# Kernel optimization log

Measured on AMD Instinct MI355X. Metric: run time of the kernel, lower is better.

## Reference

```python
import jax, jax.numpy as jnp
import numpy as np

N = 50000
E = 500000
D = 128      # input_nf = output_nf = hidden_nf
EPS = 1e-8
MAX_TRANS = 10.0


def setup_inputs() -> dict:
    key = jax.random.key(0)
    ks = jax.random.split(key, 16)
    s = lambda k, shp: jax.random.normal(k, shp, dtype=jnp.float32) * 0.05
    inp = {
        "h": jax.random.normal(ks[0], (N, D), dtype=jnp.float32),
        "edge_index": jax.random.randint(ks[1], (2, E), 0, N, dtype=jnp.int64),
        "coord": jax.random.normal(ks[2], (N, 3), dtype=jnp.float32),
        # edge_mlp: Linear(2D+1 -> D), SiLU, Linear(D -> D), SiLU
        "We1": s(ks[3], (2 * D + 1, D)), "be1": jnp.zeros((D,), jnp.float32),
        "We2": s(ks[4], (D, D)),         "be2": jnp.zeros((D,), jnp.float32),
        # att_mlp: Linear(D -> 1), Sigmoid
        "Watt": s(ks[5], (D, 1)), "batt": jnp.zeros((1,), jnp.float32),
        # coord_mlp: Linear(D -> D), SiLU, Linear(D -> 1, bias=False, xavier gain=0.001)
        "Wc1": s(ks[6], (D, D)), "bc1": jnp.zeros((D,), jnp.float32),
        "Wc2": s(ks[7], (D, 1)) * 0.001,
        # node_mlp: Linear(2D -> D), SiLU, Linear(D -> D)
        "Wn1": s(ks[8], (2 * D, D)), "bn1": jnp.zeros((D,), jnp.float32),
        "Wn2": s(ks[9], (D, D)),     "bn2": jnp.zeros((D,), jnp.float32),
    }
    return inp


def _segment_mean(data, seg_ids, num_segments):
    tot = jax.ops.segment_sum(data, seg_ids, num_segments=num_segments)
    cnt = jax.ops.segment_sum(jnp.ones_like(data), seg_ids, num_segments=num_segments)
    return tot / jnp.clip(cnt, 1.0, None)


def reference(h, edge_index, coord, We1, be1, We2, be2, Watt, batt,
              Wc1, bc1, Wc2, Wn1, bn1, Wn2, bn2):
    row, col = edge_index[0], edge_index[1]

    # coord2radial (normalize=False)
    coord_diff = coord[row] - coord[col]                      # [E, 3]
    radial = jnp.sum(coord_diff ** 2, axis=1, keepdims=True)  # [E, 1]

    # edge_model with attention
    e_in = jnp.concatenate([h[row], h[col], radial], axis=1)  # [E, 2D+1]
    e = jax.nn.silu(e_in @ We1 + be1)
    edge_feat = jax.nn.silu(e @ We2 + be2)                    # [E, D]
    att = jax.nn.sigmoid(edge_feat @ Watt + batt)             # [E, 1]
    edge_feat = edge_feat * att

    # coord_model (update_coords=True, coords_agg='mean', tanh=False)
    cw = jax.nn.silu(edge_feat @ Wc1 + bc1) @ Wc2             # [E, 1]
    trans = jnp.clip(coord_diff * cw, -MAX_TRANS, MAX_TRANS)  # [E, 3]
    agg_c = jnp.clip(_segment_mean(trans, row, N), -MAX_TRANS, MAX_TRANS)
    coord_out = coord + agg_c

    # node_model (residual=True)
    agg = jax.ops.segment_sum(edge_feat, row, num_segments=N)  # [N, D]
    n_in = jnp.concatenate([h, agg], axis=1)                   # [N, 2D]
    h_out = h + (jax.nn.silu(n_in @ Wn1 + bn1) @ Wn2 + bn2)

    return h_out, coord_out, edge_feat
```

## Files before the change

### kernel.cpp

```cpp
#include <hip/hip_runtime.h>

typedef unsigned short ushort_t;
typedef __attribute__((ext_vector_type(8))) short short8;
typedef __attribute__((ext_vector_type(4))) float f32x4;

#define NN 50000
#define EE 500000
#define DD 128
#define MAXT 10.0f

#define MFMA(a,b,c) __builtin_amdgcn_mfma_f32_16x16x32_bf16((a),(b),(c),0,0,0)

__device__ __forceinline__ ushort_t f2bf(float x){
  unsigned u = __float_as_uint(x);
  u += 0x7FFFu + ((u>>16)&1u);
  return (ushort_t)(u>>16);
}
__device__ __forceinline__ float sigm(float x){ return 1.0f/(1.0f+__expf(-x)); }
__device__ __forceinline__ float siluf(float x){ return x*sigm(x); }
__device__ __forceinline__ float clamp10(float x){ return fminf(fmaxf(x,-MAXT),MAXT); }

__device__ __forceinline__ short8 ldcvt(const float* p){
  f32x4 x = *(const f32x4*)p;
  f32x4 y = *(const f32x4*)(p+4);
  short8 t;
  #pragma unroll
  for (int j=0;j<4;++j){ t[j]=(short)f2bf(x[j]); t[j+4]=(short)f2bf(y[j]); }
  return t;
}

__global__ void k_prep(const float* __restrict__ We1, const float* __restrict__ We2,
                       const float* __restrict__ Wc1, const float* __restrict__ Wn1,
                       const float* __restrict__ Wn2, ushort_t* __restrict__ wpre)
{
  int idx = blockIdx.x*256 + threadIdx.x;
  if (idx >= 7*16384) return;
  int mat = idx >> 14;
  int loc = idx & 16383;
  int n = loc >> 7;
  int kidx = loc & 127;
  int ko = 16*(kidx&7) + (kidx>>3);
  float v;
  switch(mat){
    case 0: v = We1[kidx*DD + n]; break;
    case 1: v = We1[(128+kidx)*DD + n]; break;
    case 2: v = We2[ko*DD + n]; break;
    case 3: v = Wc1[ko*DD + n]; break;
    case 4: v = Wn1[kidx*DD + n]; break;
    case 5: v = Wn1[(128+kidx)*DD + n]; break;
    default: v = Wn2[ko*DD + n]; break;
  }
  int byteoff = n*256 + ((kidx*2) ^ ((n&7)<<4));
  *(ushort_t*)((char*)wpre + (size_t)mat*32768 + byteoff) = f2bf(v);
}

__global__ void k_zero(int* __restrict__ cnt){
  int i = blockIdx.x*256 + threadIdx.x;
  if (i < NN) cnt[i] = 0;
}
__global__ void k_count(const int* __restrict__ eidx, int* __restrict__ cnt){
  int e = blockIdx.x*256 + threadIdx.x;
  if (e < EE) atomicAdd(&cnt[eidx[e]], 1);
}
#define SCAN_B 196
__global__ void k_bsum(const int* __restrict__ cnt, int* __restrict__ bsum){
  __shared__ int sh[256];
  int t = threadIdx.x;
  int i = blockIdx.x*256 + t;
  sh[t] = (i < NN) ? cnt[i] : 0;
  __syncthreads();
  for (int off=128; off>0; off>>=1){
    if (t < off) sh[t] += sh[t+off];
    __syncthreads();
  }
  if (t==0) bsum[blockIdx.x] = sh[0];
}
__global__ void k_bscan(const int* __restrict__ bsum, int* __restrict__ boff){
  __shared__ int sh[256];
  int t = threadIdx.x;
  sh[t] = (t < SCAN_B) ? bsum[t] : 0;
  __syncthreads();
  for (int off=1; off<256; off<<=1){
    int x = (t>=off) ? sh[t-off] : 0;
    __syncthreads();
    sh[t] += x;
    __syncthreads();
  }
  if (t < SCAN_B) boff[t] = (t>0) ? sh[t-1] : 0;
}
__global__ void k_rscan(const int* __restrict__ cnt, const int* __restrict__ boff,
                        int* __restrict__ rowstart, int* __restrict__ cursor){
  __shared__ int sh[256];
  int t = threadIdx.x;
  int i = blockIdx.x*256 + t;
  int v = (i < NN) ? cnt[i] : 0;
  sh[t] = v;
  __syncthreads();
  for (int off=1; off<256; off<<=1){
    int x = (t>=off) ? sh[t-off] : 0;
    __syncthreads();
    sh[t] += x;
    __syncthreads();
  }
  int excl = sh[t] - v + boff[blockIdx.x];
  if (i < NN){ rowstart[i] = excl; cursor[i] = excl; }
  if (i == 0) rowstart[NN] = EE;
}
__global__ void k_scatter(const int* __restrict__ eidx, int* __restrict__ cursor,
                          int* __restrict__ csr){
  int e = blockIdx.x*256 + threadIdx.x;
  if (e < EE){
    int p = atomicAdd(&cursor[eidx[e]], 1);
    csr[p] = e;
  }
}

__device__ __forceinline__ void gemm_lds8(const ushort_t* ebuf, const ushort_t* Wbuf,
                                          int wv, int q, int s, f32x4 acc[8])
{
  #pragma unroll
  for (int kc=0;kc<4;++kc){
    const int koff = ((kc*64+q*16) ^ ((s&7)<<4));
    short8 a0 = *(const short8*)((const char*)ebuf + (wv*16+s)*256 + koff);
    #pragma unroll
    for (int ct=0;ct<8;++ct){
      short8 bf = *(const short8*)((const char*)Wbuf + (ct*16+s)*256 + koff);
      acc[ct] = MFMA(a0,bf,acc[ct]);
    }
  }
}
__device__ __forceinline__ void gemm_regA8(const short8 af[4], const ushort_t* Wbuf,
                                           int q, int s, f32x4 acc[8])
{
  #pragma unroll
  for (int kc=0;kc<4;++kc){
    const int koff = ((kc*64+q*16) ^ ((s&7)<<4));
    #pragma unroll
    for (int ct=0;ct<8;++ct){
      short8 bf = *(const short8*)((const char*)Wbuf + (ct*16+s)*256 + koff);
      acc[ct] = MFMA(af[kc],bf,acc[ct]);
    }
  }
}
__device__ __forceinline__ void zacc8(f32x4 acc[8]){
  #pragma unroll
  for (int b=0;b<8;++b) acc[b] = (f32x4){0.f,0.f,0.f,0.f};
}

__launch_bounds__(512,4)
__global__ void k_edge(const float* __restrict__ h,
                       const int* __restrict__ eidx,
                       const float* __restrict__ coord,
                       const float* __restrict__ We1,
                       const float* __restrict__ be1,
                       const float* __restrict__ be2,
                       const float* __restrict__ Watt,
                       const float* __restrict__ batt,
                       const float* __restrict__ bc1,
                       const float* __restrict__ Wc2,
                       const ushort_t* __restrict__ wpre,
                       float* __restrict__ ef_out,
                       float* __restrict__ trans)
{
  __shared__ ushort_t Wbuf[16384];
  __shared__ ushort_t ebuf[16384];
  const int tid = threadIdx.x;
  const int wv = tid>>6, ln = tid&63;
  const int q = ln>>4, s = ln&15;
  const int we0 = blockIdx.x*128 + wv*16;
  const int* rowI = eidx;
  const int* colI = eidx + EE;

  const int eM = min(we0 + (ln&15), EE-1);
  const int rM = rowI[eM], cM = colI[eM];
  const float cdx = coord[rM*3+0]-coord[cM*3+0];
  const float cdy = coord[rM*3+1]-coord[cM*3+1];
  const float cdz = coord[rM*3+2]-coord[cM*3+2];
  const float radial = cdx*cdx+cdy*cdy+cdz*cdz;

  const int eS0 = min(we0 + s, EE-1);
  const int nR0 = rowI[eS0], nC0 = colI[eS0];

  f32x4 acc[8];
  zacc8(acc);
  short8 af[4];

  #pragma unroll
  for (int kc=0;kc<4;++kc)
    af[kc] = ldcvt(h + (size_t)nR0*DD + kc*32 + q*8);
  { const f32x4* src=(const f32x4*)(wpre); f32x4* dst=(f32x4*)Wbuf;
    #pragma unroll
    for(int i=0;i<4;++i) dst[tid+512*i]=src[tid+512*i]; }
  __syncthreads();
  gemm_regA8(af, Wbuf, q, s, acc);

  #pragma unroll
  for (int kc=0;kc<4;++kc)
    af[kc] = ldcvt(h + (size_t)nC0*DD + kc*32 + q*8);
  __syncthreads();
  { const f32x4* src=(const f32x4*)(wpre+16384); f32x4* dst=(f32x4*)Wbuf;
    #pragma unroll
    for(int i=0;i<4;++i) dst[tid+512*i]=src[tid+512*i]; }
  __syncthreads();
  gemm_regA8(af, Wbuf, q, s, acc);

  {
    float wr[8], bb[8];
    #pragma unroll
    for (int t=0;t<8;++t){ wr[t]=We1[256*DD + 16*t+s]; bb[t]=be1[16*t+s]; }
    #pragma unroll
    for (int r=0;r<4;++r){
      int mloc = q*4 + r;
      float rad = __shfl(radial, mloc);
      short8 pk;
      #pragma unroll
      for (int t=0;t<8;++t){
        float v = siluf(acc[t][r] + rad*wr[t] + bb[t]);
        pk[t]=(short)f2bf(v);
      }
      int m = wv*16 + mloc;
      *(short8*)((char*)ebuf + m*256 + ((s*16) ^ ((m&7)<<4))) = pk;
    }
  }
  zacc8(acc);
  __syncthreads();
  { const f32x4* src=(const f32x4*)(wpre+2*16384); f32x4* dst=(f32x4*)Wbuf;
    #pragma unroll
    for(int i=0;i<4;++i) dst[tid+512*i]=src[tid+512*i]; }
  __syncthreads();

  gemm_lds8(ebuf, Wbuf, wv, q, s, acc);
  {
    float wa[8], bb[8];
    #pragma unroll
    for (int t=0;t<8;++t){ wa[t]=Watt[16*t+s]; bb[t]=be2[16*t+s]; }
    const float bat = batt[0];
    #pragma unroll
    for (int r=0;r<4;++r){
      #pragma unroll
      for (int t=0;t<8;++t) acc[t][r] = siluf(acc[t][r] + bb[t]);
      float p=0.f;
      #pragma unroll
      for (int t=0;t<8;++t) p += acc[t][r]*wa[t];
      p += __shfl_xor(p,1); p += __shfl_xor(p,2);
      p += __shfl_xor(p,4); p += __shfl_xor(p,8);
      const float att = sigm(p + bat);
      #pragma unroll
      for (int t=0;t<8;++t) acc[t][r] *= att;
    }
    #pragma unroll
    for (int r=0;r<4;++r){
      int mloc = q*4 + r;
      int e = we0 + mloc;
      short8 pk;
      #pragma unroll
      for (int t=0;t<8;++t) pk[t]=(short)f2bf(acc[t][r]);
      int m = wv*16 + mloc;
      *(short8*)((char*)ebuf + m*256 + ((s*16) ^ ((m&7)<<4))) = pk;
      if (e < EE){
        float* rp = ef_out + (size_t)e*DD + s;
        #pragma unroll
        for (int t=0;t<8;++t) rp[16*t] = acc[t][r];
      }
    }
  }
  zacc8(acc);
  __syncthreads();
  { const f32x4* src=(const f32x4*)(wpre+3*16384); f32x4* dst=(f32x4*)Wbuf;
    #pragma unroll
    for(int i=0;i<4;++i) dst[tid+512*i]=src[tid+512*i]; }
  __syncthreads();

  gemm_lds8(ebuf, Wbuf, wv, q, s, acc);
  {
    float wc[8], bb[8];
    #pragma unroll
    for (int t=0;t<8;++t){ wc[t]=Wc2[16*t+s]; bb[t]=bc1[16*t+s]; }
    #pragma unroll
    for (int r=0;r<4;++r){
      float p=0.f;
      #pragma unroll
      for (int t=0;t<8;++t) p += siluf(acc[t][r]+bb[t])*wc[t];
      p += __shfl_xor(p,1); p += __shfl_xor(p,2);
      p += __shfl_xor(p,4); p += __shfl_xor(p,8);
      int mloc = q*4 + r;
      int e = we0 + mloc;
      float dx = __shfl(cdx, mloc), dy = __shfl(cdy, mloc), dz = __shfl(cdz, mloc);
      if (e < EE && s == 0){
        trans[(size_t)e*3+0] = clamp10(dx*p);
        trans[(size_t)e*3+1] = clamp10(dy*p);
        trans[(size_t)e*3+2] = clamp10(dz*p);
      }
    }
  }
}

__launch_bounds__(256)
__global__ void k_agg(const float* __restrict__ ef,
                      const float* __restrict__ trans,
                      const int* __restrict__ rowstart,
                      const int* __restrict__ csr,
                      const float* __restrict__ coord,
                      float* __restrict__ agg,
                      float* __restrict__ coord_out)
{
  const int wv = threadIdx.x>>6, ln = threadIdx.x&63;
  const int n = blockIdx.x*4 + wv;
  if (n >= NN) return;
  const int rs = rowstart[n], re = rowstart[n+1];
  const int deg = re - rs;
  const int half = ln>>5, l4 = (ln&31)*4;
  float a0=0,a1=0,a2=0,a3=0;
  for (int j=half; j<deg; j+=2){
    const float* p = ef + (size_t)csr[rs+j]*DD + l4;
    f32x4 v = *(const f32x4*)p;
    a0+=v[0]; a1+=v[1]; a2+=v[2]; a3+=v[3];
  }
  a0 += __shfl_xor(a0,32); a1 += __shfl_xor(a1,32);
  a2 += __shfl_xor(a2,32); a3 += __shfl_xor(a3,32);
  if (half==0){
    f32x4 o = {a0,a1,a2,a3};
    *(f32x4*)(agg + (size_t)n*DD + l4) = o;
  }
  float tx=0,ty=0,tz=0;
  for (int j=ln;j<deg;j+=64){
    const float* t = trans + (size_t)csr[rs+j]*3;
    tx+=t[0]; ty+=t[1]; tz+=t[2];
  }
  #pragma unroll
  for (int m=1;m<64;m<<=1){
    tx+=__shfl_xor(tx,m); ty+=__shfl_xor(ty,m); tz+=__shfl_xor(tz,m);
  }
  if (ln==0){
    const float inv = 1.0f/(float)max(deg,1);
    coord_out[(size_t)n*3+0] = coord[(size_t)n*3+0] + clamp10(tx*inv);
    coord_out[(size_t)n*3+1] = coord[(size_t)n*3+1] + clamp10(ty*inv);
    coord_out[(size_t)n*3+2] = coord[(size_t)n*3+2] + clamp10(tz*inv);
  }
}

__launch_bounds__(512,4)
__global__ void k_node(const float* __restrict__ h,
                       const float* __restrict__ agg,
                       const ushort_t* __restrict__ wpre,
                       const float* __restrict__ bn1,
                       const float* __restrict__ bn2,
                       float* __restrict__ hout)
{
  __shared__ ushort_t Wbuf[16384];
  __shared__ ushort_t ubuf[16384];
  const int tid = threadIdx.x;
  const int wv = tid>>6, ln = tid&63;
  const int q = ln>>4, s = ln&15;
  const int n0 = blockIdx.x*128 + wv*16;
  const int nd0 = min(n0 + s, NN-1);

  f32x4 acc[8];
  zacc8(acc);
  short8 af[4];

  #pragma unroll
  for (int kc=0;kc<4;++kc)
    af[kc] = ldcvt(h + (size_t)nd0*DD + kc*32 + q*8);
  { const f32x4* src=(const f32x4*)(wpre+4*16384); f32x4* dst=(f32x4*)Wbuf;
    #pragma unroll
    for(int i=0;i<4;++i) dst[tid+512*i]=src[tid+512*i]; }
  __syncthreads();
  gemm_regA8(af, Wbuf, q, s, acc);

  #pragma unroll
  for (int kc=0;kc<4;++kc)
    af[kc] = ldcvt(agg + (size_t)nd0*DD + kc*32 + q*8);
  __syncthreads();
  { const f32x4* src=(const f32x4*)(wpre+5*16384); f32x4* dst=(f32x4*)Wbuf;
    #pragma unroll
    for(int i=0;i<4;++i) dst[tid+512*i]=src[tid+512*i]; }
  __syncthreads();
  gemm_regA8(af, Wbuf, q, s, acc);

  {
    float bb[8];
    #pragma unroll
    for (int t=0;t<8;++t) bb[t]=bn1[16*t+s];
    #pragma unroll
    for (int r=0;r<4;++r){
      int mloc = q*4 + r;
      short8 pk;
      #pragma unroll
      for (int t=0;t<8;++t) pk[t]=(short)f2bf(siluf(acc[t][r]+bb[t]));
      int m = wv*16 + mloc;
      *(short8*)((char*)ubuf + m*256 + ((s*16) ^ ((m&7)<<4))) = pk;
    }
  }
  zacc8(acc);
  __syncthreads();
  { const f32x4* src=(const f32x4*)(wpre+6*16384); f32x4* dst=(f32x4*)Wbuf;
    #pragma unroll
    for(int i=0;i<4;++i) dst[tid+512*i]=src[tid+512*i]; }
  __syncthreads();

  gemm_lds8(ubuf, Wbuf, wv, q, s, acc);

  {
    float bb[8];
    #pragma unroll
    for (int t=0;t<8;++t) bb[t]=bn2[16*t+s];
    #pragma unroll
    for (int r=0;r<4;++r){
      int n = n0 + q*4 + r;
      if (n < NN){
        const float* hp = h + (size_t)n*DD + s;
        float* op = hout + (size_t)n*DD + s;
        #pragma unroll
        for (int t=0;t<8;++t) op[16*t] = hp[16*t] + acc[t][r] + bb[t];
      }
    }
  }
}

extern "C" void kernel_launch(void* const* d_in, const int* in_sizes, int n_in,
                              void* d_out, int out_size, void* d_ws, size_t ws_size,
                              hipStream_t stream)
{
  const float* h    = (const float*)d_in[0];
  const int*   eidx = (const int*)  d_in[1];
  const float* coord= (const float*)d_in[2];
  const float* We1  = (const float*)d_in[3];
  const float* be1  = (const float*)d_in[4];
  const float* We2  = (const float*)d_in[5];
  const float* be2  = (const float*)d_in[6];
  const float* Watt = (const float*)d_in[7];
  const float* batt = (const float*)d_in[8];
  const float* Wc1  = (const float*)d_in[9];
  const float* bc1  = (const float*)d_in[10];
  const float* Wc2  = (const float*)d_in[11];
  const float* Wn1  = (const float*)d_in[12];
  const float* bn1  = (const float*)d_in[13];
  const float* Wn2  = (const float*)d_in[14];
  const float* bn2  = (const float*)d_in[15];

  float* hout     = (float*)d_out;
  float* coordout = hout + (size_t)NN*DD;
  float* efout    = coordout + (size_t)NN*3;

  char* ws = (char*)d_ws;
  float* trans   = (float*)(ws);
  float* agg     = (float*)(ws + 6000000);
  int*   cnt     = (int*)  (ws + 31600000);
  int*   cursor  = (int*)  (ws + 31800000);
  int*   rowstart= (int*)  (ws + 32000000);
  int*   csr     = (int*)  (ws + 32200064);
  ushort_t* wpre = (ushort_t*)(ws + 34200064);
  int*   bsum    = csr;
  int*   boff    = csr + 256;

  k_prep   <<<448, 256, 0, stream>>>(We1, We2, Wc1, Wn1, Wn2, wpre);
  k_zero   <<<196, 256, 0, stream>>>(cnt);
  k_count  <<<1954,256, 0, stream>>>(eidx, cnt);
  k_bsum   <<<196, 256, 0, stream>>>(cnt, bsum);
  k_bscan  <<<1,   256, 0, stream>>>(bsum, boff);
  k_rscan  <<<196, 256, 0, stream>>>(cnt, boff, rowstart, cursor);
  k_scatter<<<1954,256, 0, stream>>>(eidx, cursor, csr);
  k_edge   <<<3907,512, 0, stream>>>(h, eidx, coord, We1, be1, be2, Watt, batt,
                                     bc1, Wc2, wpre, efout, trans);
  k_agg    <<<12500,256,0, stream>>>(efout, trans, rowstart, csr, coord, agg, coordout);
  k_node   <<<391, 512, 0, stream>>>(h, agg, wpre, bn1, bn2, hout);
}
```

Before: 660.4 us.

## Pre-convert h and agg to bf16 and retile GEMMs to 32x64 warp tiles

Adds a kernel that converts h to bf16 once, so the edge kernel gathers half the bytes per row and does no per-gather conversion. The aggregation kernel now writes agg in bf16 for the same reason. The edge and node GEMMs are retiled so each wave computes a 32x64 tile instead of 16x128, which reuses each B fragment across two M tiles and cuts LDS B reads. Row reductions that now span two waves go through a small shared scratch array with extra barriers. The bf16 agg adds rounding error before the node MLP.

```diff
diff --git a/kernel.cpp b/kernel.cpp
--- a/kernel.cpp
+++ b/kernel.cpp
@@ -2,6 +2,7 @@
 
 typedef unsigned short ushort_t;
 typedef __attribute__((ext_vector_type(8))) short short8;
+typedef __attribute__((ext_vector_type(4))) short short4v;
 typedef __attribute__((ext_vector_type(4))) float f32x4;
 
 #define NN 50000
@@ -19,15 +20,6 @@
 __device__ __forceinline__ float sigm(float x){ return 1.0f/(1.0f+__expf(-x)); }
 __device__ __forceinline__ float siluf(float x){ return x*sigm(x); }
 __device__ __forceinline__ float clamp10(float x){ return fminf(fmaxf(x,-MAXT),MAXT); }
-
-__device__ __forceinline__ short8 ldcvt(const float* p){
-  f32x4 x = *(const f32x4*)p;
-  f32x4 y = *(const f32x4*)(p+4);
-  short8 t;
-  #pragma unroll
-  for (int j=0;j<4;++j){ t[j]=(short)f2bf(x[j]); t[j+4]=(short)f2bf(y[j]); }
-  return t;
-}
 
 __global__ void k_prep(const float* __restrict__ We1, const float* __restrict__ We2,
                        const float* __restrict__ Wc1, const float* __restrict__ Wn1,
@@ -54,6 +46,18 @@
   *(ushort_t*)((char*)wpre + (size_t)mat*32768 + byteoff) = f2bf(v);
 }
 
+__global__ void k_hprep(const float* __restrict__ h, ushort_t* __restrict__ hb)
+{
+  int i = blockIdx.x*256 + threadIdx.x;
+  if (i >= NN*DD/8) return;
+  f32x4 x = ((const f32x4*)h)[2*i];
+  f32x4 y = ((const f32x4*)h)[2*i+1];
+  short8 t;
+  #pragma unroll
+  for (int j=0;j<4;++j){ t[j]=(short)f2bf(x[j]); t[j+4]=(short)f2bf(y[j]); }
+  ((short8*)hb)[i] = t;
+}
+
 __global__ void k_zero(int* __restrict__ cnt){
   int i = blockIdx.x*256 + threadIdx.x;
   if (i < NN) cnt[i] = 0;
@@ -115,40 +119,54 @@
   }
 }
 
-__device__ __forceinline__ void gemm_lds8(const ushort_t* ebuf, const ushort_t* Wbuf,
-                                          int wv, int q, int s, f32x4 acc[8])
+__device__ __forceinline__ void stage(const ushort_t* __restrict__ wpre, int mat,
+                                      ushort_t* Wbuf, int tid)
+{
+  const f32x4* src = (const f32x4*)(wpre + (size_t)mat*16384);
+  f32x4* dst = (f32x4*)Wbuf;
+  #pragma unroll
+  for (int i=0;i<4;++i) dst[tid + 512*i] = src[tid + 512*i];
+}
+__device__ __forceinline__ void zacc(f32x4 acc[2][4]){
+  #pragma unroll
+  for (int i=0;i<2;++i)
+    #pragma unroll
+    for (int j=0;j<4;++j) acc[i][j] = (f32x4){0.f,0.f,0.f,0.f};
+}
+__device__ __forceinline__ void gemm_b16(const short8 af[2][4], const ushort_t* Wbuf,
+                                         int cbase, int q, int s, f32x4 acc[2][4])
 {
   #pragma unroll
   for (int kc=0;kc<4;++kc){
     const int koff = ((kc*64+q*16) ^ ((s&7)<<4));
-    short8 a0 = *(const short8*)((const char*)ebuf + (wv*16+s)*256 + koff);
-    #pragma unroll
-    for (int ct=0;ct<8;++ct){
-      short8 bf = *(const short8*)((const char*)Wbuf + (ct*16+s)*256 + koff);
-      acc[ct] = MFMA(a0,bf,acc[ct]);
-    }
-  }
-}
-__device__ __forceinline__ void gemm_regA8(const short8 af[4], const ushort_t* Wbuf,
-                                           int q, int s, f32x4 acc[8])
+    #pragma unroll
+    for (int ct=0;ct<4;++ct){
+      short8 bf = *(const short8*)((const char*)Wbuf + (cbase+ct*16+s)*256 + koff);
+      acc[0][ct] = MFMA(af[0][kc],bf,acc[0][ct]);
+      acc[1][ct] = MFMA(af[1][kc],bf,acc[1][ct]);
+    }
+  }
+}
+__device__ __forceinline__ void gemm_lds16(const ushort_t* ebuf, const ushort_t* Wbuf,
+                                           int mbase, int cbase, int q, int s,
+                                           f32x4 acc[2][4])
 {
   #pragma unroll
   for (int kc=0;kc<4;++kc){
     const int koff = ((kc*64+q*16) ^ ((s&7)<<4));
-    #pragma unroll
-    for (int ct=0;ct<8;++ct){
-      short8 bf = *(const short8*)((const char*)Wbuf + (ct*16+s)*256 + koff);
-      acc[ct] = MFMA(af[kc],bf,acc[ct]);
-    }
-  }
-}
-__device__ __forceinline__ void zacc8(f32x4 acc[8]){
-  #pragma unroll
-  for (int b=0;b<8;++b) acc[b] = (f32x4){0.f,0.f,0.f,0.f};
+    short8 a0 = *(const short8*)((const char*)ebuf + (mbase+s)*256 + koff);
+    short8 a1 = *(const short8*)((const char*)ebuf + (mbase+16+s)*256 + koff);
+    #pragma unroll
+    for (int ct=0;ct<4;++ct){
+      short8 bf = *(const short8*)((const char*)Wbuf + (cbase+ct*16+s)*256 + koff);
+      acc[0][ct] = MFMA(a0,bf,acc[0][ct]);
+      acc[1][ct] = MFMA(a1,bf,acc[1][ct]);
+    }
+  }
 }
 
 __launch_bounds__(512,4)
-__global__ void k_edge(const float* __restrict__ h,
+__global__ void k_edge(const ushort_t* __restrict__ hb,
                        const int* __restrict__ eidx,
                        const float* __restrict__ coord,
                        const float* __restrict__ We1,
@@ -164,133 +182,152 @@
 {
   __shared__ ushort_t Wbuf[16384];
   __shared__ ushort_t ebuf[16384];
+  __shared__ float dscr[128][2];
   const int tid = threadIdx.x;
   const int wv = tid>>6, ln = tid&63;
+  const int wm = wv&3, wn = wv>>2;
   const int q = ln>>4, s = ln&15;
-  const int we0 = blockIdx.x*128 + wv*16;
+  const int cbase = wn*64;
+  const int we0 = blockIdx.x*128;
+  const int mb = wm*32;
   const int* rowI = eidx;
   const int* colI = eidx + EE;
 
-  const int eM = min(we0 + (ln&15), EE-1);
+  const int eM = min(we0 + mb + (ln&31), EE-1);
   const int rM = rowI[eM], cM = colI[eM];
   const float cdx = coord[rM*3+0]-coord[cM*3+0];
   const float cdy = coord[rM*3+1]-coord[cM*3+1];
   const float cdz = coord[rM*3+2]-coord[cM*3+2];
   const float radial = cdx*cdx+cdy*cdy+cdz*cdz;
 
-  const int eS0 = min(we0 + s, EE-1);
-  const int nR0 = rowI[eS0], nC0 = colI[eS0];
-
-  f32x4 acc[8];
-  zacc8(acc);
-  short8 af[4];
-
-  #pragma unroll
-  for (int kc=0;kc<4;++kc)
-    af[kc] = ldcvt(h + (size_t)nR0*DD + kc*32 + q*8);
-  { const f32x4* src=(const f32x4*)(wpre); f32x4* dst=(f32x4*)Wbuf;
-    #pragma unroll
-    for(int i=0;i<4;++i) dst[tid+512*i]=src[tid+512*i]; }
-  __syncthreads();
-  gemm_regA8(af, Wbuf, q, s, acc);
-
-  #pragma unroll
-  for (int kc=0;kc<4;++kc)
-    af[kc] = ldcvt(h + (size_t)nC0*DD + kc*32 + q*8);
-  __syncthreads();
-  { const f32x4* src=(const f32x4*)(wpre+16384); f32x4* dst=(f32x4*)Wbuf;
-    #pragma unroll
-    for(int i=0;i<4;++i) dst[tid+512*i]=src[tid+512*i]; }
-  __syncthreads();
-  gemm_regA8(af, Wbuf, q, s, acc);
+  const int eS0 = min(we0 + mb + s,      EE-1);
+  const int eS1 = min(we0 + mb + 16 + s, EE-1);
+  const int nR0 = rowI[eS0], nR1 = rowI[eS1];
+  const int nC0 = colI[eS0], nC1 = colI[eS1];
+
+  f32x4 acc[2][4];
+  short8 af[2][4];
+  zacc(acc);
+
+  #pragma unroll
+  for (int kc=0;kc<4;++kc){
+    af[0][kc] = *(const short8*)(hb + (size_t)nR0*DD + kc*32 + q*8);
+    af[1][kc] = *(const short8*)(hb + (size_t)nR1*DD + kc*32 + q*8);
+  }
+  stage(wpre, 0, Wbuf, tid);
+  __syncthreads();
+  gemm_b16(af, Wbuf, cbase, q, s, acc);
+
+  #pragma unroll
+  for (int kc=0;kc<4;++kc){
+    af[0][kc] = *(const short8*)(hb + (size_t)nC0*DD + kc*32 + q*8);
+    af[1][kc] = *(const short8*)(hb + (size_t)nC1*DD + kc*32 + q*8);
+  }
+  __syncthreads();
+  stage(wpre, 1, Wbuf, tid);
+  __syncthreads();
+  gemm_b16(af, Wbuf, cbase, q, s, acc);
 
   {
-    float wr[8], bb[8];
-    #pragma unroll
-    for (int t=0;t<8;++t){ wr[t]=We1[256*DD + 16*t+s]; bb[t]=be1[16*t+s]; }
-    #pragma unroll
-    for (int r=0;r<4;++r){
-      int mloc = q*4 + r;
-      float rad = __shfl(radial, mloc);
-      short8 pk;
+    float wr[4], bb[4];
+    #pragma unroll
+    for (int ct=0;ct<4;++ct){ wr[ct]=We1[256*DD + cbase+16*ct+s]; bb[ct]=be1[cbase+16*ct+s]; }
+    #pragma unroll
+    for (int mt=0;mt<2;++mt){
       #pragma unroll
-      for (int t=0;t<8;++t){
-        float v = siluf(acc[t][r] + rad*wr[t] + bb[t]);
-        pk[t]=(short)f2bf(v);
+      for (int r=0;r<4;++r){
+        int mloc = mt*16 + q*4 + r;
+        float rad = __shfl(radial, mloc);
+        short4v pk;
+        #pragma unroll
+        for (int ct=0;ct<4;++ct) pk[ct]=(short)f2bf(siluf(acc[mt][ct][r] + rad*wr[ct] + bb[ct]));
+        int m = mb + mloc;
+        *(short4v*)((char*)ebuf + m*256 + ((16*s+8*wn) ^ ((m&7)<<4))) = pk;
       }
-      int m = wv*16 + mloc;
-      *(short8*)((char*)ebuf + m*256 + ((s*16) ^ ((m&7)<<4))) = pk;
-    }
-  }
-  zacc8(acc);
-  __syncthreads();
-  { const f32x4* src=(const f32x4*)(wpre+2*16384); f32x4* dst=(f32x4*)Wbuf;
-    #pragma unroll
-    for(int i=0;i<4;++i) dst[tid+512*i]=src[tid+512*i]; }
-  __syncthreads();
-
-  gemm_lds8(ebuf, Wbuf, wv, q, s, acc);
+    }
+  }
+  zacc(acc);
+  __syncthreads();
+  stage(wpre, 2, Wbuf, tid);
+  __syncthreads();
+
+  gemm_lds16(ebuf, Wbuf, mb, cbase, q, s, acc);
   {
-    float wa[8], bb[8];
-    #pragma unroll
-    for (int t=0;t<8;++t){ wa[t]=Watt[16*t+s]; bb[t]=be2[16*t+s]; }
+    float wa[4], bb[4];
+    #pragma unroll
+    for (int ct=0;ct<4;++ct){ wa[ct]=Watt[cbase+16*ct+s]; bb[ct]=be2[cbase+16*ct+s]; }
+    #pragma unroll
+    for (int mt=0;mt<2;++mt){
+      #pragma unroll
+      for (int r=0;r<4;++r){
+        float p = 0.f;
+        #pragma unroll
+        for (int ct=0;ct<4;++ct){
+          float v = siluf(acc[mt][ct][r] + bb[ct]);
+          acc[mt][ct][r] = v;
+          p += v*wa[ct];
+        }
+        p += __shfl_xor(p,1); p += __shfl_xor(p,2);
+        p += __shfl_xor(p,4); p += __shfl_xor(p,8);
+        if (s==0) dscr[mb + mt*16 + q*4 + r][wn] = p;
+      }
+    }
+  }
+  __syncthreads();
+  stage(wpre, 3, Wbuf, tid);
+  {
     const float bat = batt[0];
     #pragma unroll
-    for (int r=0;r<4;++r){
+    for (int mt=0;mt<2;++mt){
       #pragma unroll
-      for (int t=0;t<8;++t) acc[t][r] = siluf(acc[t][r] + bb[t]);
-      float p=0.f;
+      for (int r=0;r<4;++r){
+        int m = mb + mt*16 + q*4 + r;
+        float att = sigm(dscr[m][0] + dscr[m][1] + bat);
+        short4v pk;
+        #pragma unroll
+        for (int ct=0;ct<4;++ct){
+          acc[mt][ct][r] *= att;
+          pk[ct]=(short)f2bf(acc[mt][ct][r]);
+        }
+        *(short4v*)((char*)ebuf + m*256 + ((16*s+8*wn) ^ ((m&7)<<4))) = pk;
+        int e = we0 + m;
+        if (e < EE){
+          float* rp = ef_out + (size_t)e*DD + cbase + s;
+          #pragma unroll
+          for (int ct=0;ct<4;++ct) rp[16*ct] = acc[mt][ct][r];
+        }
+      }
+    }
+  }
+  zacc(acc);
+  __syncthreads();
+
+  gemm_lds16(ebuf, Wbuf, mb, cbase, q, s, acc);
+  {
+    float wc[4], bb[4];
+    #pragma unroll
+    for (int ct=0;ct<4;++ct){ wc[ct]=Wc2[cbase+16*ct+s]; bb[ct]=bc1[cbase+16*ct+s]; }
+    #pragma unroll
+    for (int mt=0;mt<2;++mt){
       #pragma unroll
-      for (int t=0;t<8;++t) p += acc[t][r]*wa[t];
-      p += __shfl_xor(p,1); p += __shfl_xor(p,2);
-      p += __shfl_xor(p,4); p += __shfl_xor(p,8);
-      const float att = sigm(p + bat);
-      #pragma unroll
-      for (int t=0;t<8;++t) acc[t][r] *= att;
-    }
-    #pragma unroll
-    for (int r=0;r<4;++r){
-      int mloc = q*4 + r;
-      int e = we0 + mloc;
-      short8 pk;
-      #pragma unroll
-      for (int t=0;t<8;++t) pk[t]=(short)f2bf(acc[t][r]);
-      int m = wv*16 + mloc;
-      *(short8*)((char*)ebuf + m*256 + ((s*16) ^ ((m&7)<<4))) = pk;
-      if (e < EE){
-        float* rp = ef_out + (size_t)e*DD + s;
+      for (int r=0;r<4;++r){
+        float p = 0.f;
         #pragma unroll
-        for (int t=0;t<8;++t) rp[16*t] = acc[t][r];
+        for (int ct=0;ct<4;++ct) p += siluf(acc[mt][ct][r]+bb[ct])*wc[ct];
+        p += __shfl_xor(p,1); p += __shfl_xor(p,2);
+        p += __shfl_xor(p,4); p += __shfl_xor(p,8);
+        if (s==0) dscr[mb + mt*16 + q*4 + r][wn] = p;
       }
     }
   }
-  zacc8(acc);
-  __syncthreads();
-  { const f32x4* src=(const f32x4*)(wpre+3*16384); f32x4* dst=(f32x4*)Wbuf;
-    #pragma unroll
-    for(int i=0;i<4;++i) dst[tid+512*i]=src[tid+512*i]; }
-  __syncthreads();
-
-  gemm_lds8(ebuf, Wbuf, wv, q, s, acc);
-  {
-    float wc[8], bb[8];
-    #pragma unroll
-    for (int t=0;t<8;++t){ wc[t]=Wc2[16*t+s]; bb[t]=bc1[16*t+s]; }
-    #pragma unroll
-    for (int r=0;r<4;++r){
-      float p=0.f;
-      #pragma unroll
-      for (int t=0;t<8;++t) p += siluf(acc[t][r]+bb[t])*wc[t];
-      p += __shfl_xor(p,1); p += __shfl_xor(p,2);
-      p += __shfl_xor(p,4); p += __shfl_xor(p,8);
-      int mloc = q*4 + r;
-      int e = we0 + mloc;
-      float dx = __shfl(cdx, mloc), dy = __shfl(cdy, mloc), dz = __shfl(cdz, mloc);
-      if (e < EE && s == 0){
-        trans[(size_t)e*3+0] = clamp10(dx*p);
-        trans[(size_t)e*3+1] = clamp10(dy*p);
-        trans[(size_t)e*3+2] = clamp10(dz*p);
-      }
+  __syncthreads();
+  if (wn==0 && ln<32){
+    int e = we0 + mb + ln;
+    if (e < EE){
+      float p = dscr[mb+ln][0] + dscr[mb+ln][1];
+      trans[(size_t)e*3+0] = clamp10(cdx*p);
+      trans[(size_t)e*3+1] = clamp10(cdy*p);
+      trans[(size_t)e*3+2] = clamp10(cdz*p);
     }
   }
 }
@@ -301,7 +338,7 @@
                       const int* __restrict__ rowstart,
                       const int* __restrict__ csr,
                       const float* __restrict__ coord,
-                      float* __restrict__ agg,
+                      ushort_t* __restrict__ aggb,
                       float* __restrict__ coord_out)
 {
   const int wv = threadIdx.x>>6, ln = threadIdx.x&63;
@@ -319,8 +356,8 @@
   a0 += __shfl_xor(a0,32); a1 += __shfl_xor(a1,32);
   a2 += __shfl_xor(a2,32); a3 += __shfl_xor(a3,32);
   if (half==0){
-    f32x4 o = {a0,a1,a2,a3};
-    *(f32x4*)(agg + (size_t)n*DD + l4) = o;
+    short4v o = { (short)f2bf(a0),(short)f2bf(a1),(short)f2bf(a2),(short)f2bf(a3) };
+    *(short4v*)(aggb + (size_t)n*DD + l4) = o;
   }
   float tx=0,ty=0,tz=0;
   for (int j=ln;j<deg;j+=64){
@@ -341,7 +378,8 @@
 
 __launch_bounds__(512,4)
 __global__ void k_node(const float* __restrict__ h,
-                       const float* __restrict__ agg,
+                       const ushort_t* __restrict__ hb,
+                       const ushort_t* __restrict__ aggb,
                        const ushort_t* __restrict__ wpre,
                        const float* __restrict__ bn1,
                        const float* __restrict__ bn2,
@@ -351,68 +389,75 @@
   __shared__ ushort_t ubuf[16384];
   const int tid = threadIdx.x;
   const int wv = tid>>6, ln = tid&63;
+  const int wm = wv&3, wn = wv>>2;
   const int q = ln>>4, s = ln&15;
-  const int n0 = blockIdx.x*128 + wv*16;
-  const int nd0 = min(n0 + s, NN-1);
-
-  f32x4 acc[8];
-  zacc8(acc);
-  short8 af[4];
-
-  #pragma unroll
-  for (int kc=0;kc<4;++kc)
-    af[kc] = ldcvt(h + (size_t)nd0*DD + kc*32 + q*8);
-  { const f32x4* src=(const f32x4*)(wpre+4*16384); f32x4* dst=(f32x4*)Wbuf;
-    #pragma unroll
-    for(int i=0;i<4;++i) dst[tid+512*i]=src[tid+512*i]; }
-  __syncthreads();
-  gemm_regA8(af, Wbuf, q, s, acc);
-
-  #pragma unroll
-  for (int kc=0;kc<4;++kc)
-    af[kc] = ldcvt(agg + (size_t)nd0*DD + kc*32 + q*8);
-  __syncthreads();
-  { const f32x4* src=(const f32x4*)(wpre+5*16384); f32x4* dst=(f32x4*)Wbuf;
-    #pragma unroll
-    for(int i=0;i<4;++i) dst[tid+512*i]=src[tid+512*i]; }
-  __syncthreads();
-  gemm_regA8(af, Wbuf, q, s, acc);
+  const int cbase = wn*64;
+  const int n0 = blockIdx.x*128;
+  const int mb = wm*32;
+  const int nd0 = min(n0 + mb + s,      NN-1);
+  const int nd1 = min(n0 + mb + 16 + s, NN-1);
+
+  f32x4 acc[2][4];
+  short8 af[2][4];
+  zacc(acc);
+
+  #pragma unroll
+  for (int kc=0;kc<4;++kc){
+    af[0][kc] = *(const short8*)(hb + (size_t)nd0*DD + kc*32 + q*8);
+    af[1][kc] = *(const short8*)(hb + (size_t)nd1*DD + kc*32 + q*8);
+  }
+  stage(wpre, 4, Wbuf, tid);
+  __syncthreads();
+  gemm_b16(af, Wbuf, cbase, q, s, acc);
+
+  #pragma unroll
+  for (int kc=0;kc<4;++kc){
+    af[0][kc] = *(const short8*)(aggb + (size_t)nd0*DD + kc*32 + q*8);
+    af[1][kc] = *(const short8*)(aggb + (size_t)nd1*DD + kc*32 + q*8);
+  }
+  __syncthreads();
+  stage(wpre, 5, Wbuf, tid);
+  __syncthreads();
+  gemm_b16(af, Wbuf, cbase, q, s, acc);
 
   {
-    float bb[8];
-    #pragma unroll
-    for (int t=0;t<8;++t) bb[t]=bn1[16*t+s];
-    #pragma unroll
-    for (int r=0;r<4;++r){
-      int mloc = q*4 + r;
-      short8 pk;
+    float bb[4];
+    #pragma unroll
+    for (int ct=0;ct<4;++ct) bb[ct]=bn1[cbase+16*ct+s];
+    #pragma unroll
+    for (int mt=0;mt<2;++mt){
       #pragma unroll
-      for (int t=0;t<8;++t) pk[t]=(short)f2bf(siluf(acc[t][r]+bb[t]));
-      int m = wv*16 + mloc;
-      *(short8*)((char*)ubuf + m*256 + ((s*16) ^ ((m&7)<<4))) = pk;
-    }
-  }
-  zacc8(acc);
-  __syncthreads();
-  { const f32x4* src=(const f32x4*)(wpre+6*16384); f32x4* dst=(f32x4*)Wbuf;
-    #pragma unroll
-    for(int i=0;i<4;++i) dst[tid+512*i]=src[tid+512*i]; }
-  __syncthreads();
-
-  gemm_lds8(ubuf, Wbuf, wv, q, s, acc);
+      for (int r=0;r<4;++r){
+        int m = mb + mt*16 + q*4 + r;
+        short4v pk;
+        #pragma unroll
+        for (int ct=0;ct<4;++ct) pk[ct]=(short)f2bf(siluf(acc[mt][ct][r]+bb[ct]));
+        *(short4v*)((char*)ubuf + m*256 + ((16*s+8*wn) ^ ((m&7)<<4))) = pk;
+      }
+    }
+  }
+  zacc(acc);
+  __syncthreads();
+  stage(wpre, 6, Wbuf, tid);
+  __syncthreads();
+
+  gemm_lds16(ubuf, Wbuf, mb, cbase, q, s, acc);
 
   {
-    float bb[8];
-    #pragma unroll
-    for (int t=0;t<8;++t) bb[t]=bn2[16*t+s];
-    #pragma unroll
-    for (int r=0;r<4;++r){
-      int n = n0 + q*4 + r;
-      if (n < NN){
-        const float* hp = h + (size_t)n*DD + s;
-        float* op = hout + (size_t)n*DD + s;
-        #pragma unroll
-        for (int t=0;t<8;++t) op[16*t] = hp[16*t] + acc[t][r] + bb[t];
+    float bb[4];
+    #pragma unroll
+    for (int ct=0;ct<4;++ct) bb[ct]=bn2[cbase+16*ct+s];
+    #pragma unroll
+    for (int mt=0;mt<2;++mt){
+      #pragma unroll
+      for (int r=0;r<4;++r){
+        int n = n0 + mb + mt*16 + q*4 + r;
+        if (n < NN){
+          const float* hp = h + (size_t)n*DD + cbase + s;
+          float* op = hout + (size_t)n*DD + cbase + s;
+          #pragma unroll
+          for (int ct=0;ct<4;++ct) op[16*ct] = hp[16*ct] + acc[mt][ct][r] + bb[ct];
+        }
       }
     }
   }
@@ -444,8 +489,9 @@
   float* efout    = coordout + (size_t)NN*3;
 
   char* ws = (char*)d_ws;
-  float* trans   = (float*)(ws);
-  float* agg     = (float*)(ws + 6000000);
+  float*    trans = (float*)(ws);
+  ushort_t* aggb  = (ushort_t*)(ws + 6000000);
+  ushort_t* hb    = (ushort_t*)(ws + 18800000);
   int*   cnt     = (int*)  (ws + 31600000);
   int*   cursor  = (int*)  (ws + 31800000);
   int*   rowstart= (int*)  (ws + 32000000);
@@ -455,14 +501,15 @@
   int*   boff    = csr + 256;
 
   k_prep   <<<448, 256, 0, stream>>>(We1, We2, Wc1, Wn1, Wn2, wpre);
+  k_hprep  <<<3125,256, 0, stream>>>(h, hb);
   k_zero   <<<196, 256, 0, stream>>>(cnt);
   k_count  <<<1954,256, 0, stream>>>(eidx, cnt);
   k_bsum   <<<196, 256, 0, stream>>>(cnt, bsum);
   k_bscan  <<<1,   256, 0, stream>>>(bsum, boff);
   k_rscan  <<<196, 256, 0, stream>>>(cnt, boff, rowstart, cursor);
   k_scatter<<<1954,256, 0, stream>>>(eidx, cursor, csr);
-  k_edge   <<<3907,512, 0, stream>>>(h, eidx, coord, We1, be1, be2, Watt, batt,
+  k_edge   <<<3907,512, 0, stream>>>(hb, eidx, coord, We1, be1, be2, Watt, batt,
                                      bc1, Wc2, wpre, efout, trans);
-  k_agg    <<<12500,256,0, stream>>>(efout, trans, rowstart, csr, coord, agg, coordout);
-  k_node   <<<391, 512, 0, stream>>>(h, agg, wpre, bn1, bn2, hout);
-}
+  k_agg    <<<12500,256,0, stream>>>(efout, trans, rowstart, csr, coord, aggb, coordout);
+  k_node   <<<391, 512, 0, stream>>>(h, hb, aggb, wpre, bn1, bn2, hout);
+}
```

After: 655.0 us. About the same (-0.8%).
